# Kernel tuning notes

Hardware: AMD Instinct MI355X
Metric: run time of the kernel (lower is better)

## Reference

```python
import jax, jax.numpy as jnp
import numpy as np

N_NODES = 50000
N_EDGES = 600000
D = 128

def _linear_params(key, fan_in, fan_out):
    # torch nn.Linear default init: U(-1/sqrt(fan_in), 1/sqrt(fan_in))
    k1, k2 = jax.random.split(key)
    bound = 1.0 / np.sqrt(fan_in)
    W = jax.random.uniform(k1, (fan_in, fan_out), minval=-bound, maxval=bound, dtype=jnp.float32)
    b = jax.random.uniform(k2, (fan_out,), minval=-bound, maxval=bound, dtype=jnp.float32)
    return W, b

def setup_inputs() -> dict:
    key = jax.random.key(0)
    kh, ke, k1, k2, k3, k4 = jax.random.split(key, 6)
    h = jax.random.normal(kh, (N_NODES, D), dtype=jnp.float32)
    edges = jax.random.randint(ke, (N_EDGES, 2), 0, N_NODES, dtype=jnp.int32)
    msg_W1, msg_b1 = _linear_params(k1, 2 * D, D)
    msg_W2, msg_b2 = _linear_params(k2, D, D)
    upd_W1, upd_b1 = _linear_params(k3, 2 * D, D)
    upd_W2, upd_b2 = _linear_params(k4, D, D)
    return {"h": h, "edges": edges,
            "msg_W1": msg_W1, "msg_b1": msg_b1, "msg_W2": msg_W2, "msg_b2": msg_b2,
            "upd_W1": upd_W1, "upd_b1": upd_b1, "upd_W2": upd_W2, "upd_b2": upd_b2}

def reference(h, edges, msg_W1, msg_b1, msg_W2, msg_b2, upd_W1, upd_b1, upd_W2, upd_b2):
    src = edges[:, 0]
    dst = edges[:, 1]
    # message MLP over concatenated [h_src, h_dst] per edge: [E, 2D] -> [E, D]
    pair = jnp.concatenate([h[src], h[dst]], axis=-1)
    msg = jax.nn.relu(pair @ msg_W1 + msg_b1) @ msg_W2 + msg_b2
    # scatter-add aggregate messages onto destination nodes: [N, D]
    agg = jax.ops.segment_sum(msg, dst, num_segments=h.shape[0])
    # update MLP on [h, agg]: [N, 2D] -> [N, D]
    upd_in = jnp.concatenate([h, agg], axis=-1)
    h_new = jax.nn.relu(upd_in @ upd_W1 + upd_b1) @ upd_W2 + upd_b2
    return h + h_new
```

## Files before the change

kernel.cpp:

```cpp
#include <hip/hip_runtime.h>
#include <hip/hip_bf16.h>

#define NN 50000
#define NE 600000
#define TN 64
#define NT ((NN + TN - 1) / TN)
#define CAP 1024

typedef unsigned short u16;
typedef unsigned int u32;
typedef unsigned long long u64;
typedef __attribute__((ext_vector_type(8))) short bf16x8;
typedef __attribute__((ext_vector_type(16))) float f32x16;
typedef __attribute__((ext_vector_type(4))) int int4v;

#define SM_AB   0
#define SM_MSGT 16384
#define SM_TT   32768
#define SM_ST   49152
#define SM_S0   57344
#define SM_S1   65536
#define SM_BIAS 73728
#define SMEM_TOTAL 74752

__device__ __forceinline__ void bar_lds() {
    asm volatile("s_waitcnt lgkmcnt(0)" ::: "memory");
    __builtin_amdgcn_s_barrier();
}

__device__ __forceinline__ u16 f2b(float x) {
    __hip_bfloat16 b = __float2bfloat16(x);
    union { __hip_bfloat16 b; u16 u; } c; c.b = b; return c.u;
}
__device__ __forceinline__ int4v zero4() {
    int4v v; v[0]=0; v[1]=0; v[2]=0; v[3]=0; return v;
}
__device__ __forceinline__ f32x16 zero16() {
    f32x16 z;
#pragma unroll
    for (int i = 0; i < 16; ++i) z[i] = 0.f;
    return z;
}
__device__ __forceinline__ int4v cvt8(const float* __restrict__ p) {
    const float4* q = (const float4*)p;
    float4 f0 = q[0], f1 = q[1];
    union { u16 u[8]; int4v v; } r;
    r.u[0]=f2b(f0.x); r.u[1]=f2b(f0.y); r.u[2]=f2b(f0.z); r.u[3]=f2b(f0.w);
    r.u[4]=f2b(f1.x); r.u[5]=f2b(f1.y); r.u[6]=f2b(f1.z); r.u[7]=f2b(f1.w);
    return r.v;
}
__device__ __forceinline__ u64 pack4(float a, float b, float c, float d) {
    union { u16 u[4]; u64 q; } r;
    r.u[0]=f2b(a); r.u[1]=f2b(b); r.u[2]=f2b(c); r.u[3]=f2b(d); return r.q;
}
__device__ __forceinline__ f32x16 mfma16(bf16x8 a, bf16x8 b, f32x16 c) {
    return __builtin_amdgcn_mfma_f32_32x32x16_bf16(a, b, c, 0, 0, 0);
}
__device__ __forceinline__ bf16x8 ld256(const char* base, int row, int c) {
    return *(const bf16x8*)(base + row * 256 + ((c ^ (row & 15)) << 4));
}
__device__ __forceinline__ bf16x8 ld128r(const char* base, int row, int c) {
    return *(const bf16x8*)(base + row * 128 + ((c ^ (row & 7)) << 4));
}

__global__ void prep_kernel(const float* __restrict__ h,
                            const float* __restrict__ W1m, const float* __restrict__ W2m,
                            const float* __restrict__ W1u, const float* __restrict__ W2u,
                            u16* __restrict__ w1tm, u16* __restrict__ w2tm,
                            u16* __restrict__ w1tu, u16* __restrict__ w2tu,
                            u16* __restrict__ hbuf, int do_h)
{
    int tid = blockIdx.x * blockDim.x + threadIdx.x;
    int stride = gridDim.x * blockDim.x;
    for (int i = tid; i < 128 * 256; i += stride) {
        int n = i >> 8, k = i & 255;
        w1tm[i] = f2b(W1m[k * 128 + n]);
        w1tu[i] = f2b(W1u[k * 128 + n]);
    }
    for (int i = tid; i < 128 * 128; i += stride) {
        int n = i >> 7, k = i & 127;
        w2tm[i] = f2b(W2m[k * 128 + n]);
        w2tu[i] = f2b(W2u[k * 128 + n]);
    }
    if (do_h) {
        for (int i = tid; i < NN * 128 / 8; i += stride)
            *(int4v*)(hbuf + (size_t)i * 8) = cvt8(h + (size_t)i * 8);
    }
}

__global__ __launch_bounds__(256) void scatter_kernel(
    const int* __restrict__ edges, u32* __restrict__ elist, int* __restrict__ cursor)
{
    __shared__ int lcnt[NT];
    const int e0 = blockIdx.x * 2048;
    for (int i = threadIdx.x; i < NT; i += 256) lcnt[i] = 0;
    __syncthreads();
#pragma unroll
    for (int k = 0; k < 8; ++k) {
        int e = e0 + k * 256 + threadIdx.x;
        if (e < NE) atomicAdd(&lcnt[edges[2 * e + 1] >> 6], 1);
    }
    __syncthreads();
    for (int i = threadIdx.x; i < NT; i += 256) {
        int cn = lcnt[i];
        if (cn > 0) lcnt[i] = atomicAdd(&cursor[i], cn);
    }
    __syncthreads();
#pragma unroll
    for (int k = 0; k < 8; ++k) {
        int e = e0 + k * 256 + threadIdx.x;
        if (e < NE) {
            int s = edges[2 * e], d = edges[2 * e + 1];
            int bin = d >> 6;
            int pos = atomicAdd(&lcnt[bin], 1);
            if (pos < CAP) elist[(size_t)bin * CAP + pos] = (u32)s | ((u32)(d & 63) << 16);
        }
    }
}

__global__ __launch_bounds__(256, 2) void fused_kernel(
    const float* __restrict__ h, const u16* __restrict__ hb, int use_hb,
    const u32* __restrict__ elist, const int* __restrict__ cursor,
    const u16* __restrict__ w1m, const u16* __restrict__ w2m,
    const u16* __restrict__ w1u, const u16* __restrict__ w2u,
    const float* __restrict__ b1m, const float* __restrict__ b2m,
    const float* __restrict__ b1u, const float* __restrict__ b2u,
    float* __restrict__ outp)
{
    extern __shared__ char sm[];
    char* ab   = sm + SM_AB;
    char* msgt = sm + SM_MSGT;
    char* tt   = sm + SM_TT;
    char* Stb  = sm + SM_ST;
    char* S0   = sm + SM_S0;
    char* S1   = sm + SM_S1;
    char* bias = sm + SM_BIAS;
    char* htu  = sm + SM_ST;

    const int tid  = threadIdx.x;
    const int lane = tid & 63;
    const int wid  = tid >> 6;
    const int l31  = lane & 31;
    const int kg   = lane >> 5;
    const int nrow  = wid * 32 + l31;
    const int ecol0 = l31;
    const int ecol1 = 32 + l31;

    const int bin = blockIdx.x;
    const int n0  = bin * TN;
    int size = cursor[bin]; if (size > CAP) size = CAP;
    const u32* el = elist + (size_t)bin * CAP;
    const int nchunk = (size + 63) >> 6;

    bf16x8 w1f[8], w2f[8];
#pragma unroll
    for (int kk = 0; kk < 8; ++kk) {
        w1f[kk] = *(const bf16x8*)(w1m + nrow * 256 + (kk * 2 + kg) * 8);
        w2f[kk] = *(const bf16x8*)(w2m + nrow * 128 + (kk * 2 + kg) * 8);
    }
    const float b2ms = b2m[nrow];

    for (int i = tid; i < 1024; i += 256) {
        int row = i >> 4, c = i & 15;
        int node = n0 + row;
        int4v v = zero4();
        if (node < NN) {
            if (use_hb) v = *(const int4v*)(hb + (size_t)node * 128 + c * 8);
            else        v = cvt8(h + (size_t)node * 128 + c * 8);
        }
        *(int4v*)(msgt + row * 256 + ((c ^ (row & 15)) << 4)) = v;
    }
    if (tid < 32)      *(float4*)(bias + tid * 16)          = ((const float4*)b1m)[tid];
    else if (tid < 64) *(float4*)(bias + 512 + (tid-32)*16) = ((const float4*)b1u)[tid - 32];
    {
        char* z = sm + SM_ST + tid * 64;
        *(int4v*)z = zero4(); *(int4v*)(z + 16) = zero4();
        *(int4v*)(z + 32) = zero4(); *(int4v*)(z + 48) = zero4();
    }

    auto put_St = [&](u32 rec, int cb2, u16 val) {
        if (cb2 + lane < size) {
            int d = (int)((rec >> 16) & 63);
            *(u16*)(Stb + lane * 128 + (((d >> 3) ^ (lane & 7)) << 4) + (d & 7) * 2) = val;
        }
    };
    auto put_S = [&](char* Sbuf, u32 rec, int cb2) {
        if (cb2 + lane < size) {
            int d = (int)((rec >> 16) & 63);
            *(u16*)(Sbuf + d * 128 + (((lane >> 3) ^ (d & 7)) << 4) + (lane & 7) * 2) = 0x3F80;
        }
    };

    const int s_row0 = tid >> 4, s_cc = tid & 15;
    auto stage_load = [&](u32 dle_c, int cb2, int4v* v) {
#pragma unroll
        for (int u = 0; u < 4; ++u) {
            int row = s_row0 + 16 * u;
            int s = ((int)__shfl((int)dle_c, row, 64)) & 0xFFFF;
            v[u] = zero4();
            if (cb2 + row < size)
                v[u] = use_hb ? *(const int4v*)(hb + (size_t)s * 128 + s_cc * 8)
                              : cvt8(h + (size_t)s * 128 + s_cc * 8);
        }
    };
    auto stage_write = [&](const int4v* v) {
#pragma unroll
        for (int u = 0; u < 4; ++u) {
            int row = s_row0 + 16 * u;
            *(int4v*)(ab + row * 256 + ((s_cc ^ (row & 15)) << 4)) = v[u];
        }
    };

    u32 dle = (lane < size) ? el[lane] : 0u;
    if (nchunk > 0) {
        int4v v[4];
        stage_load(dle, 0, v);
        stage_write(v);
    }
    __syncthreads();

    {
        f32x16 t0 = zero16(), t1 = zero16();
        __builtin_amdgcn_s_setprio(1);
#pragma unroll
        for (int kk = 0; kk < 8; ++kk) {
            bf16x8 wtf = *(const bf16x8*)(w1m + nrow * 256 + (16 + kk * 2 + kg) * 8);
            int ch = kk * 2 + kg;
            t0 = mfma16(wtf, ld256(msgt, ecol0, ch), t0);
            t1 = mfma16(wtf, ld256(msgt, ecol1, ch), t1);
        }
        __builtin_amdgcn_s_setprio(0);
#pragma unroll
        for (int r = 0; r < 16; ++r) {
            int n1 = wid * 32 + (r & 3) + 8 * (r >> 2) + 4 * kg;
            *(u16*)(tt + n1 * 128 + (((ecol0 >> 3) ^ (n1 & 7)) << 4) + (ecol0 & 7) * 2) = f2b(t0[r]);
            *(u16*)(tt + n1 * 128 + (((ecol1 >> 3) ^ (n1 & 7)) << 4) + (ecol1 & 7) * 2) = f2b(t1[r]);
        }
    }
    if (wid == 0) { put_St(dle, 0, 0x3F80); put_S(S0, dle, 0); }
    bar_lds();

    f32x16 aggT0 = zero16(), aggT1 = zero16();
    for (int c = 0; c < nchunk; ++c) {
        const int cb = c << 6;
        const bool havepf = (c + 1 < nchunk);
        char* Scur = (c & 1) ? S1 : S0;
        char* Snxt = (c & 1) ? S0 : S1;

        u32 dle_next = (havepf && (cb + 64 + lane < size)) ? el[cb + 64 + lane] : 0u;

        f32x16 mm0 = zero16(), mm1 = zero16();
        __builtin_amdgcn_s_setprio(1);
#pragma unroll
        for (int kk = 0; kk < 4; ++kk) {
            int ch = kk * 2 + kg;
            bf16x8 ttf = ld128r(tt, nrow, ch);
            mm0 = mfma16(ttf, ld128r(Stb, ecol0, ch), mm0);
            mm1 = mfma16(ttf, ld128r(Stb, ecol1, ch), mm1);
        }
#pragma unroll
        for (int kk = 0; kk < 8; ++kk) {
            int ch = kk * 2 + kg;
            mm0 = mfma16(w1f[kk], ld256(ab, ecol0, ch), mm0);
            mm1 = mfma16(w1f[kk], ld256(ab, ecol1, ch), mm1);
        }
        __builtin_amdgcn_s_setprio(0);
        bar_lds();

        int4v v[4];
        if (havepf) stage_load(dle_next, cb + 64, v);
#pragma unroll
        for (int rq = 0; rq < 4; ++rq) {
            float4 bq = *(const float4*)(bias + (wid * 32 + 8 * rq + 4 * kg) * 4);
            int cch = wid * 4 + rq;
            u64 q0 = pack4(fmaxf(mm0[4 * rq + 0] + bq.x, 0.f),
                           fmaxf(mm0[4 * rq + 1] + bq.y, 0.f),
                           fmaxf(mm0[4 * rq + 2] + bq.z, 0.f),
                           fmaxf(mm0[4 * rq + 3] + bq.w, 0.f));
            u64 q1 = pack4(fmaxf(mm1[4 * rq + 0] + bq.x, 0.f),
                           fmaxf(mm1[4 * rq + 1] + bq.y, 0.f),
                           fmaxf(mm1[4 * rq + 2] + bq.z, 0.f),
                           fmaxf(mm1[4 * rq + 3] + bq.w, 0.f));
            *(u64*)(ab + ecol0 * 256 + ((cch ^ (ecol0 & 15)) << 4) + 8 * kg) = q0;
            *(u64*)(ab + ecol1 * 256 + ((cch ^ (ecol1 & 15)) << 4) + 8 * kg) = q1;
        }
        if (havepf) {
            char* z = Snxt + tid * 32;
            *(int4v*)z = zero4(); *(int4v*)(z + 16) = zero4();
            if (wid == 0) {
                put_St(dle, cb, 0);
                asm volatile("s_waitcnt lgkmcnt(0)" ::: "memory");
                put_St(dle_next, cb + 64, 0x3F80);
            }
        }
        bar_lds();

        {
            f32x16 c20 = zero16(), c21 = zero16();
            __builtin_amdgcn_s_setprio(1);
#pragma unroll
            for (int kk = 0; kk < 8; ++kk) {
                int ch = kk * 2 + kg;
                c20 = mfma16(ld256(ab, ecol0, ch), w2f[kk], c20);
                c21 = mfma16(ld256(ab, ecol1, ch), w2f[kk], c21);
            }
            __builtin_amdgcn_s_setprio(0);
#pragma unroll
            for (int rq = 0; rq < 4; ++rq) {
                u64 q0 = pack4(c20[4 * rq + 0] + b2ms, c20[4 * rq + 1] + b2ms,
                               c20[4 * rq + 2] + b2ms, c20[4 * rq + 3] + b2ms);
                u64 q1 = pack4(c21[4 * rq + 0] + b2ms, c21[4 * rq + 1] + b2ms,
                               c21[4 * rq + 2] + b2ms, c21[4 * rq + 3] + b2ms);
                *(u64*)(msgt + nrow * 128 + ((rq ^ (nrow & 7)) << 4) + 8 * kg) = q0;
                *(u64*)(msgt + nrow * 128 + (((4 + rq) ^ (nrow & 7)) << 4) + 8 * kg) = q1;
            }
        }
        if (wid == 0 && havepf) put_S(Snxt, dle_next, cb + 64);
        bar_lds();

        __builtin_amdgcn_s_setprio(1);
#pragma unroll
        for (int kk = 0; kk < 4; ++kk) {
            int ch = kk * 2 + kg;
            bf16x8 msf = ld128r(msgt, nrow, ch);
            aggT0 = mfma16(msf, ld128r(Scur, ecol0, ch), aggT0);
            aggT1 = mfma16(msf, ld128r(Scur, ecol1, ch), aggT1);
        }
        __builtin_amdgcn_s_setprio(0);
        if (havepf) stage_write(v);
        bar_lds();
        dle = dle_next;
    }

#pragma unroll
    for (int rq = 0; rq < 4; ++rq) {
        int cch = wid * 4 + rq;
        u64 q0 = pack4(aggT0[4 * rq + 0], aggT0[4 * rq + 1], aggT0[4 * rq + 2], aggT0[4 * rq + 3]);
        u64 q1 = pack4(aggT1[4 * rq + 0], aggT1[4 * rq + 1], aggT1[4 * rq + 2], aggT1[4 * rq + 3]);
        *(u64*)(ab + ecol0 * 256 + ((cch ^ (ecol0 & 15)) << 4) + 8 * kg) = q0;
        *(u64*)(ab + ecol1 * 256 + ((cch ^ (ecol1 & 15)) << 4) + 8 * kg) = q1;
    }
    for (int i = tid; i < 1024; i += 256) {
        int row = i >> 4, c = i & 15;
        int node = n0 + row;
        int4v v = zero4();
        if (node < NN) {
            if (use_hb) v = *(const int4v*)(hb + (size_t)node * 128 + c * 8);
            else        v = cvt8(h + (size_t)node * 128 + c * 8);
        }
        *(int4v*)(htu + row * 256 + ((c ^ (row & 15)) << 4)) = v;
    }
    bar_lds();

    {
        f32x16 au0 = zero16(), au1 = zero16();
        {
            bf16x8 wa[8];
#pragma unroll
            for (int kk = 0; kk < 8; ++kk)
                wa[kk] = *(const bf16x8*)(w1u + nrow * 256 + (kk * 2 + kg) * 8);
            __builtin_amdgcn_s_setprio(1);
#pragma unroll
            for (int kk = 0; kk < 8; ++kk) {
                int ch = kk * 2 + kg;
                au0 = mfma16(wa[kk], ld256(htu, ecol0, ch), au0);
                au1 = mfma16(wa[kk], ld256(htu, ecol1, ch), au1);
            }
            __builtin_amdgcn_s_setprio(0);
        }
        {
            bf16x8 wbf[8];
#pragma unroll
            for (int kk = 0; kk < 8; ++kk)
                wbf[kk] = *(const bf16x8*)(w1u + nrow * 256 + ((8 + kk) * 2 + kg) * 8);
            __builtin_amdgcn_s_setprio(1);
#pragma unroll
            for (int kk = 0; kk < 8; ++kk) {
                int ch = kk * 2 + kg;
                au0 = mfma16(wbf[kk], ld256(ab, ecol0, ch), au0);
                au1 = mfma16(wbf[kk], ld256(ab, ecol1, ch), au1);
            }
            __builtin_amdgcn_s_setprio(0);
        }
#pragma unroll
        for (int rq = 0; rq < 4; ++rq) {
            float4 bq = *(const float4*)(bias + 512 + (wid * 32 + 8 * rq + 4 * kg) * 4);
            int cch = wid * 4 + rq;
            u64 q0 = pack4(fmaxf(au0[4 * rq + 0] + bq.x, 0.f),
                           fmaxf(au0[4 * rq + 1] + bq.y, 0.f),
                           fmaxf(au0[4 * rq + 2] + bq.z, 0.f),
                           fmaxf(au0[4 * rq + 3] + bq.w, 0.f));
            u64 q1 = pack4(fmaxf(au1[4 * rq + 0] + bq.x, 0.f),
                           fmaxf(au1[4 * rq + 1] + bq.y, 0.f),
                           fmaxf(au1[4 * rq + 2] + bq.z, 0.f),
                           fmaxf(au1[4 * rq + 3] + bq.w, 0.f));
            *(u64*)(msgt + ecol0 * 256 + ((cch ^ (ecol0 & 15)) << 4) + 8 * kg) = q0;
            *(u64*)(msgt + ecol1 * 256 + ((cch ^ (ecol1 & 15)) << 4) + 8 * kg) = q1;
        }
    }
    bar_lds();

    {
        bf16x8 wc[8];
#pragma unroll
        for (int kk = 0; kk < 8; ++kk)
            wc[kk] = *(const bf16x8*)(w2u + nrow * 128 + (kk * 2 + kg) * 8);
        const float b2us = b2u[nrow];
        f32x16 cu0 = zero16(), cu1 = zero16();
        __builtin_amdgcn_s_setprio(1);
#pragma unroll
        for (int kk = 0; kk < 8; ++kk) {
            int ch = kk * 2 + kg;
            cu0 = mfma16(ld256(msgt, ecol0, ch), wc[kk], cu0);
            cu1 = mfma16(ld256(msgt, ecol1, ch), wc[kk], cu1);
        }
        __builtin_amdgcn_s_setprio(0);
#pragma unroll
        for (int r = 0; r < 16; ++r) {
            int rmap = (r & 3) + 8 * (r >> 2) + 4 * kg;
            int ng0 = n0 + rmap;
            int ng1 = n0 + 32 + rmap;
            if (ng0 < NN) {
                size_t o = (size_t)ng0 * 128 + nrow;
                outp[o] = cu0[r] + b2us + h[o];
            }
            if (ng1 < NN) {
                size_t o = (size_t)ng1 * 128 + nrow;
                outp[o] = cu1[r] + b2us + h[o];
            }
        }
    }
}

extern "C" void kernel_launch(void* const* d_in, const int* in_sizes, int n_in,
                              void* d_out, int out_size, void* d_ws, size_t ws_size,
                              hipStream_t stream) {
    const float* h   = (const float*)d_in[0];
    const int* edges = (const int*)d_in[1];
    const float* W1m = (const float*)d_in[2];
    const float* b1m = (const float*)d_in[3];
    const float* W2m = (const float*)d_in[4];
    const float* b2m = (const float*)d_in[5];
    const float* W1u = (const float*)d_in[6];
    const float* b1u = (const float*)d_in[7];
    const float* W2u = (const float*)d_in[8];
    const float* b2u = (const float*)d_in[9];
    float* out = (float*)d_out;

    char* ws = (char*)d_ws;
    u16* w1tm  = (u16*)(ws + 0);
    u16* w2tm  = (u16*)(ws + 65536);
    u16* w1tu  = (u16*)(ws + 98304);
    u16* w2tu  = (u16*)(ws + 163840);
    int* curs  = (int*)(ws + 196608);
    u32* elist = (u32*)(ws + 200704);
    u16* hb    = (u16*)(ws + 3403776);
    int use_hb = (ws_size >= 3403776ull + (size_t)NN * 128 * 2) ? 1 : 0;

    (void)hipFuncSetAttribute((const void*)fused_kernel,
                              hipFuncAttributeMaxDynamicSharedMemorySize, SMEM_TOTAL);

    hipMemsetAsync(curs, 0, NT * sizeof(int), stream);
    prep_kernel<<<512, 256, 0, stream>>>(h, W1m, W2m, W1u, W2u,
                                         w1tm, w2tm, w1tu, w2tu, hb, use_hb);
    scatter_kernel<<<(NE + 2047) / 2048, 256, 0, stream>>>(edges, elist, curs);
    fused_kernel<<<NT, 256, SMEM_TOTAL, stream>>>(h, hb, use_hb, elist, curs,
                                                  w1tm, w2tm, w1tu, w2tu,
                                                  b1m, b2m, b1u, b2u, out);
}
```

Baseline: 165.9 us.

## Feed message MLP output straight into scatter MFMA via register permutes

New measurement: 152.3 us. 1.09x faster.

```diff
diff --git a/kernel.cpp b/kernel.cpp
--- a/kernel.cpp
+++ b/kernel.cpp
@@ -15,13 +15,11 @@
 typedef __attribute__((ext_vector_type(4))) int int4v;
 
 #define SM_AB   0
-#define SM_MSGT 16384
-#define SM_TT   32768
-#define SM_ST   49152
-#define SM_S0   57344
-#define SM_S1   65536
-#define SM_BIAS 73728
-#define SMEM_TOTAL 74752
+#define SM_TT   16384
+#define SM_ST   32768
+#define SM_S    40960
+#define SM_BIAS 49152
+#define SMEM_TOTAL 50176
 
 __device__ __forceinline__ void bar_lds() {
     asm volatile("s_waitcnt lgkmcnt(0)" ::: "memory");
@@ -129,11 +127,9 @@
 {
     extern __shared__ char sm[];
     char* ab   = sm + SM_AB;
-    char* msgt = sm + SM_MSGT;
-    char* tt   = sm + SM_TT;
+    char* ttr  = sm + SM_TT;
     char* Stb  = sm + SM_ST;
-    char* S0   = sm + SM_S0;
-    char* S1   = sm + SM_S1;
+    char* Sb   = sm + SM_S;
     char* bias = sm + SM_BIAS;
     char* htu  = sm + SM_ST;
 
@@ -168,7 +164,7 @@
             if (use_hb) v = *(const int4v*)(hb + (size_t)node * 128 + c * 8);
             else        v = cvt8(h + (size_t)node * 128 + c * 8);
         }
-        *(int4v*)(msgt + row * 256 + ((c ^ (row & 15)) << 4)) = v;
+        *(int4v*)(ttr + row * 256 + ((c ^ (row & 15)) << 4)) = v;
     }
     if (tid < 32)      *(float4*)(bias + tid * 16)          = ((const float4*)b1m)[tid];
     else if (tid < 64) *(float4*)(bias + 512 + (tid-32)*16) = ((const float4*)b1u)[tid - 32];
@@ -184,10 +180,10 @@
             *(u16*)(Stb + lane * 128 + (((d >> 3) ^ (lane & 7)) << 4) + (d & 7) * 2) = val;
         }
     };
-    auto put_S = [&](char* Sbuf, u32 rec, int cb2) {
+    auto put_S = [&](u32 rec, int cb2, u16 val) {
         if (cb2 + lane < size) {
             int d = (int)((rec >> 16) & 63);
-            *(u16*)(Sbuf + d * 128 + (((lane >> 3) ^ (d & 7)) << 4) + (lane & 7) * 2) = 0x3F80;
+            *(u16*)(Sb + d * 128 + (((lane >> 3) ^ (d & 7)) << 4) + (lane & 7) * 2) = val;
         }
     };
 
@@ -211,6 +207,32 @@
         }
     };
 
+    auto mkfrags = [&](const f32x16& cc, bf16x8& lo, bf16x8& hi) {
+        u32 u0,u1,u2,u3,u4,u5,u6,u7;
+        {
+            float a0=cc[0]+b2ms, a1=cc[1]+b2ms, a2=cc[2]+b2ms, a3=cc[3]+b2ms;
+            float a4=cc[4]+b2ms, a5=cc[5]+b2ms, a6=cc[6]+b2ms, a7=cc[7]+b2ms;
+            float a8=cc[8]+b2ms, a9=cc[9]+b2ms, aA=cc[10]+b2ms, aB=cc[11]+b2ms;
+            float aC=cc[12]+b2ms, aD=cc[13]+b2ms, aE=cc[14]+b2ms, aF=cc[15]+b2ms;
+            asm("v_cvt_pk_bf16_f32 %0, %1, %2" : "=v"(u0) : "v"(a0), "v"(a1));
+            asm("v_cvt_pk_bf16_f32 %0, %1, %2" : "=v"(u1) : "v"(a2), "v"(a3));
+            asm("v_cvt_pk_bf16_f32 %0, %1, %2" : "=v"(u2) : "v"(a4), "v"(a5));
+            asm("v_cvt_pk_bf16_f32 %0, %1, %2" : "=v"(u3) : "v"(a6), "v"(a7));
+            asm("v_cvt_pk_bf16_f32 %0, %1, %2" : "=v"(u4) : "v"(a8), "v"(a9));
+            asm("v_cvt_pk_bf16_f32 %0, %1, %2" : "=v"(u5) : "v"(aA), "v"(aB));
+            asm("v_cvt_pk_bf16_f32 %0, %1, %2" : "=v"(u6) : "v"(aC), "v"(aD));
+            asm("v_cvt_pk_bf16_f32 %0, %1, %2" : "=v"(u7) : "v"(aE), "v"(aF));
+        }
+        asm volatile("v_permlane32_swap_b32 %0, %1" : "+v"(u0), "+v"(u2));
+        asm volatile("v_permlane32_swap_b32 %0, %1" : "+v"(u1), "+v"(u3));
+        asm volatile("v_permlane32_swap_b32 %0, %1" : "+v"(u4), "+v"(u6));
+        asm volatile("v_permlane32_swap_b32 %0, %1" : "+v"(u5), "+v"(u7));
+        union { u32 w[4]; bf16x8 v; } A, B;
+        A.w[0]=u0; A.w[1]=u1; A.w[2]=u2; A.w[3]=u3;
+        B.w[0]=u4; B.w[1]=u5; B.w[2]=u6; B.w[3]=u7;
+        lo = A.v; hi = B.v;
+    };
+
     u32 dle = (lane < size) ? el[lane] : 0u;
     if (nchunk > 0) {
         int4v v[4];
@@ -219,33 +241,34 @@
     }
     __syncthreads();
 
+    f32x16 t0 = zero16(), t1 = zero16();
     {
-        f32x16 t0 = zero16(), t1 = zero16();
         __builtin_amdgcn_s_setprio(1);
 #pragma unroll
         for (int kk = 0; kk < 8; ++kk) {
             bf16x8 wtf = *(const bf16x8*)(w1m + nrow * 256 + (16 + kk * 2 + kg) * 8);
             int ch = kk * 2 + kg;
-            t0 = mfma16(wtf, ld256(msgt, ecol0, ch), t0);
-            t1 = mfma16(wtf, ld256(msgt, ecol1, ch), t1);
+            t0 = mfma16(wtf, ld256(ttr, ecol0, ch), t0);
+            t1 = mfma16(wtf, ld256(ttr, ecol1, ch), t1);
         }
         __builtin_amdgcn_s_setprio(0);
-#pragma unroll
-        for (int r = 0; r < 16; ++r) {
-            int n1 = wid * 32 + (r & 3) + 8 * (r >> 2) + 4 * kg;
-            *(u16*)(tt + n1 * 128 + (((ecol0 >> 3) ^ (n1 & 7)) << 4) + (ecol0 & 7) * 2) = f2b(t0[r]);
-            *(u16*)(tt + n1 * 128 + (((ecol1 >> 3) ^ (n1 & 7)) << 4) + (ecol1 & 7) * 2) = f2b(t1[r]);
-        }
-    }
-    if (wid == 0) { put_St(dle, 0, 0x3F80); put_S(S0, dle, 0); }
+    }
+    if (wid == 0) { put_St(dle, 0, 0x3F80); put_S(dle, 0, 0x3F80); }
     bar_lds();
 
+#pragma unroll
+    for (int r = 0; r < 16; ++r) {
+        int n1 = wid * 32 + (r & 3) + 8 * (r >> 2) + 4 * kg;
+        *(u16*)(ttr + n1 * 128 + (((ecol0 >> 3) ^ (n1 & 7)) << 4) + (ecol0 & 7) * 2) = f2b(t0[r]);
+        *(u16*)(ttr + n1 * 128 + (((ecol1 >> 3) ^ (n1 & 7)) << 4) + (ecol1 & 7) * 2) = f2b(t1[r]);
+    }
+    bar_lds();
+
     f32x16 aggT0 = zero16(), aggT1 = zero16();
+    u32 dle_prev = 0;
     for (int c = 0; c < nchunk; ++c) {
         const int cb = c << 6;
         const bool havepf = (c + 1 < nchunk);
-        char* Scur = (c & 1) ? S1 : S0;
-        char* Snxt = (c & 1) ? S0 : S1;
 
         u32 dle_next = (havepf && (cb + 64 + lane < size)) ? el[cb + 64 + lane] : 0u;
 
@@ -254,7 +277,7 @@
 #pragma unroll
         for (int kk = 0; kk < 4; ++kk) {
             int ch = kk * 2 + kg;
-            bf16x8 ttf = ld128r(tt, nrow, ch);
+            bf16x8 ttf = ld128r(ttr, nrow, ch);
             mm0 = mfma16(ttf, ld128r(Stb, ecol0, ch), mm0);
             mm1 = mfma16(ttf, ld128r(Stb, ecol1, ch), mm1);
         }
@@ -284,14 +307,12 @@
             *(u64*)(ab + ecol0 * 256 + ((cch ^ (ecol0 & 15)) << 4) + 8 * kg) = q0;
             *(u64*)(ab + ecol1 * 256 + ((cch ^ (ecol1 & 15)) << 4) + 8 * kg) = q1;
         }
-        if (havepf) {
-            char* z = Snxt + tid * 32;
-            *(int4v*)z = zero4(); *(int4v*)(z + 16) = zero4();
-            if (wid == 0) {
-                put_St(dle, cb, 0);
-                asm volatile("s_waitcnt lgkmcnt(0)" ::: "memory");
-                put_St(dle_next, cb + 64, 0x3F80);
-            }
+        if (wid == 0) {
+            if (c > 0) put_S(dle_prev, cb - 64, 0);
+            put_St(dle, cb, 0);
+            asm volatile("s_waitcnt lgkmcnt(0)" ::: "memory");
+            put_St(dle_next, cb + 64, 0x3F80);
+            put_S(dle, cb, 0x3F80);
         }
         bar_lds();
 
@@ -305,30 +326,25 @@
                 c21 = mfma16(ld256(ab, ecol1, ch), w2f[kk], c21);
             }
             __builtin_amdgcn_s_setprio(0);
-#pragma unroll
-            for (int rq = 0; rq < 4; ++rq) {
-                u64 q0 = pack4(c20[4 * rq + 0] + b2ms, c20[4 * rq + 1] + b2ms,
-                               c20[4 * rq + 2] + b2ms, c20[4 * rq + 3] + b2ms);
-                u64 q1 = pack4(c21[4 * rq + 0] + b2ms, c21[4 * rq + 1] + b2ms,
-                               c21[4 * rq + 2] + b2ms, c21[4 * rq + 3] + b2ms);
-                *(u64*)(msgt + nrow * 128 + ((rq ^ (nrow & 7)) << 4) + 8 * kg) = q0;
-                *(u64*)(msgt + nrow * 128 + (((4 + rq) ^ (nrow & 7)) << 4) + 8 * kg) = q1;
-            }
-        }
-        if (wid == 0 && havepf) put_S(Snxt, dle_next, cb + 64);
+            bf16x8 fA, fB, fC, fD;
+            mkfrags(c20, fA, fB);
+            mkfrags(c21, fC, fD);
+            __builtin_amdgcn_s_setprio(1);
+            aggT0 = mfma16(fA, ld128r(Sb, ecol0, 0 + kg), aggT0);
+            aggT1 = mfma16(fA, ld128r(Sb, ecol1, 0 + kg), aggT1);
+            aggT0 = mfma16(fB, ld128r(Sb, ecol0, 2 + kg), aggT0);
+            aggT1 = mfma16(fB, ld128r(Sb, ecol1, 2 + kg), aggT1);
+            aggT0 = mfma16(fC, ld128r(Sb, ecol0, 4 + kg), aggT0);
+            aggT1 = mfma16(fC, ld128r(Sb, ecol1, 4 + kg), aggT1);
+            aggT0 = mfma16(fD, ld128r(Sb, ecol0, 6 + kg), aggT0);
+            aggT1 = mfma16(fD, ld128r(Sb, ecol1, 6 + kg), aggT1);
+            __builtin_amdgcn_s_setprio(0);
+        }
         bar_lds();
 
-        __builtin_amdgcn_s_setprio(1);
-#pragma unroll
-        for (int kk = 0; kk < 4; ++kk) {
-            int ch = kk * 2 + kg;
-            bf16x8 msf = ld128r(msgt, nrow, ch);
-            aggT0 = mfma16(msf, ld128r(Scur, ecol0, ch), aggT0);
-            aggT1 = mfma16(msf, ld128r(Scur, ecol1, ch), aggT1);
-        }
-        __builtin_amdgcn_s_setprio(0);
         if (havepf) stage_write(v);
         bar_lds();
+        dle_prev = dle;
         dle = dle_next;
     }
 
@@ -382,6 +398,7 @@
             }
             __builtin_amdgcn_s_setprio(0);
         }
+        bar_lds();
 #pragma unroll
         for (int rq = 0; rq < 4; ++rq) {
             float4 bq = *(const float4*)(bias + 512 + (wid * 32 + 8 * rq + 4 * kg) * 4);
@@ -394,8 +411,8 @@
                            fmaxf(au1[4 * rq + 1] + bq.y, 0.f),
                            fmaxf(au1[4 * rq + 2] + bq.z, 0.f),
                            fmaxf(au1[4 * rq + 3] + bq.w, 0.f));
-            *(u64*)(msgt + ecol0 * 256 + ((cch ^ (ecol0 & 15)) << 4) + 8 * kg) = q0;
-            *(u64*)(msgt + ecol1 * 256 + ((cch ^ (ecol1 & 15)) << 4) + 8 * kg) = q1;
+            *(u64*)(ttr + ecol0 * 256 + ((cch ^ (ecol0 & 15)) << 4) + 8 * kg) = q0;
+            *(u64*)(ttr + ecol1 * 256 + ((cch ^ (ecol1 & 15)) << 4) + 8 * kg) = q1;
         }
     }
     bar_lds();
@@ -411,8 +428,8 @@
 #pragma unroll
         for (int kk = 0; kk < 8; ++kk) {
             int ch = kk * 2 + kg;
-            cu0 = mfma16(ld256(msgt, ecol0, ch), wc[kk], cu0);
-            cu1 = mfma16(ld256(msgt, ecol1, ch), wc[kk], cu1);
+            cu0 = mfma16(ld256(ttr, ecol0, ch), wc[kk], cu0);
+            cu1 = mfma16(ld256(ttr, ecol1, ch), wc[kk], cu1);
         }
         __builtin_amdgcn_s_setprio(0);
 #pragma unroll
```
